# Kernel tuning notes

Hardware: AMD Instinct MI355X
Metric: run time of the kernel (lower is better)

The kernel has to match this reference:

```python
import jax, jax.numpy as jnp
import numpy as np

B, S, D, DFF = 4, 2048, 1024, 4096


def setup_inputs() -> dict:
    key = jax.random.key(0)
    ks = jax.random.split(key, 7)
    scale = 1.0 / np.sqrt(D)
    return {
        "x": jax.random.normal(ks[0], (B, S, D), dtype=jnp.float32),
        "wq": jax.random.normal(ks[1], (D, D), dtype=jnp.float32) * scale,
        "wk": jax.random.normal(ks[2], (D, D), dtype=jnp.float32) * scale,
        "wv": jax.random.normal(ks[3], (D, D), dtype=jnp.float32) * scale,
        "wo": jax.random.normal(ks[4], (D, D), dtype=jnp.float32) * scale,
        "w1": jax.random.normal(ks[5], (D, DFF), dtype=jnp.float32) * scale,
        "w2": jax.random.normal(ks[6], (DFF, D), dtype=jnp.float32) * (1.0 / np.sqrt(DFF)),
    }


def reference(x, wq, wk, wv, wo, w1, w2):
    # Single-head attention, NO 1/sqrt(d) scaling (faithful to source).
    q = x @ wq  # [B,S,D]
    k = x @ wk
    v = x @ wv
    scores = jnp.einsum("bsd,btd->bst", q, k)  # [B,S,S]
    weights = jax.nn.softmax(scores, axis=-1)
    attn = jnp.einsum("bst,btd->bsd", weights, v)
    proj = attn @ wo
    hidden = jax.nn.relu(proj @ w1)  # [B,S,DFF]
    out = hidden @ w2
    return out + x
```

## Files before the change

### kernel.cpp

```cpp
#include <hip/hip_runtime.h>
#include <hip/hip_bf16.h>
#include <hip/hip_fp16.h>


typedef _Float16 f16;
typedef __attribute__((ext_vector_type(8))) _Float16 f16x8;
typedef __attribute__((ext_vector_type(4))) _Float16 f16x4;
typedef __attribute__((ext_vector_type(4))) float f32x4;

#define BM 128
#define BN 128
#define BK 64

__device__ inline void gload16(const void* g, void* l) {
    __builtin_amdgcn_global_load_lds(
        (const __attribute__((address_space(1))) void*)g,
        (__attribute__((address_space(3))) void*)l, 16, 0, 0);
}

template<int EPI>
__global__ __launch_bounds__(256, 2)
void gemm_f16(const f16* __restrict__ A, const f16* __restrict__ Bt,
              const float* __restrict__ Res, void* __restrict__ Cv,
              int K, int lda, int ldb, int ldc,
              long long sA, long long sB, long long sC)
{
    __shared__ char smem[32 * 1024];
    f16* Ash = (f16*)smem;
    f16* Bsh = (f16*)(smem + 16384);
    float* xbuf = (float*)smem;

    const int t = threadIdx.x;
    const int z = blockIdx.z;
    A  += (size_t)z * sA;
    Bt += (size_t)z * sB;

    const int bm0 = blockIdx.x * BM;
    const int bn0 = blockIdx.y * BN;

    const int lane = t & 63;
    const int wid  = t >> 6;
    const int quad = lane >> 4;
    const int m16  = lane & 15;
    const int ks   = wid & 1;
    const int wn64 = (wid >> 1) * 64;

    const int r0 = t >> 3;
    const int kc = ((t & 7) ^ (r0 & 7)) * 8;
    const char* gA[4]; const char* gB[4];
    #pragma unroll
    for (int i = 0; i < 4; ++i) {
        gA[i] = (const char*)(A  + (size_t)(bm0 + i * 32 + r0) * lda + kc);
        gB[i] = (const char*)(Bt + (size_t)(bn0 + i * 32 + r0) * ldb + kc);
    }
    char* lA = (char*)Ash + (wid << 10);
    char* lB = (char*)Bsh + (wid << 10);

    f32x4 acc[8][4] = {};

    const int nk = K / BK;
    #define ISSUE(kt) do { const int ko = (kt) * 128;   \
        gload16(gA[0] + ko, lA);                        \
        gload16(gA[1] + ko, lA + 4096);                 \
        gload16(gA[2] + ko, lA + 8192);                 \
        gload16(gA[3] + ko, lA + 12288);                \
        gload16(gB[0] + ko, lB);                        \
        gload16(gB[1] + ko, lB + 4096);                 \
        gload16(gB[2] + ko, lB + 8192);                 \
        gload16(gB[3] + ko, lB + 12288); } while (0)

    const int swz = m16 & 7;
    const int ha  = ((ks * 4 + quad) ^ swz) * 8;

    ISSUE(0);
    for (int kt = 0; kt < nk; ++kt) {
        __syncthreads();
        f16x8 af[8], bf[4];
        #pragma unroll
        for (int i = 0; i < 8; ++i)
            af[i] = *(const f16x8*)&Ash[(i * 16 + m16) * BK + ha];
        #pragma unroll
        for (int j = 0; j < 4; ++j)
            bf[j] = *(const f16x8*)&Bsh[(wn64 + j * 16 + m16) * BK + ha];
        __syncthreads();
        if (kt + 1 < nk) ISSUE(kt + 1);
        #pragma unroll
        for (int i = 0; i < 8; ++i)
            #pragma unroll
            for (int j = 0; j < 4; ++j)
                acc[i][j] = __builtin_amdgcn_mfma_f32_16x16x32_f16(
                                af[i], bf[j], acc[i][j], 0, 0, 0);
    }
    #undef ISSUE

    float* xb = xbuf + (wid >> 1) * 4096;
    #define XIDX(row, col) ((row) * 64 + ((col) ^ (((row) & 4) << 2)))
    if (ks == 1) {
        #pragma unroll
        for (int i = 0; i < 4; ++i)
            #pragma unroll
            for (int j = 0; j < 4; ++j)
                #pragma unroll
                for (int ri = 0; ri < 4; ++ri)
                    xb[XIDX(i * 16 + quad * 4 + ri, j * 16 + m16)] = acc[i][j][ri];
    }
    __syncthreads();
    if (ks == 0) {
        #pragma unroll
        for (int i = 0; i < 4; ++i)
            #pragma unroll
            for (int j = 0; j < 4; ++j)
                #pragma unroll
                for (int ri = 0; ri < 4; ++ri)
                    acc[i][j][ri] += xb[XIDX(i * 16 + quad * 4 + ri, j * 16 + m16)];
    }
    __syncthreads();
    if (ks == 0) {
        #pragma unroll
        for (int i = 0; i < 4; ++i)
            #pragma unroll
            for (int j = 0; j < 4; ++j)
                #pragma unroll
                for (int ri = 0; ri < 4; ++ri)
                    xb[XIDX(i * 16 + quad * 4 + ri, j * 16 + m16)] = acc[i + 4][j][ri];
    }
    __syncthreads();
    if (ks == 1) {
        #pragma unroll
        for (int i = 0; i < 4; ++i)
            #pragma unroll
            for (int j = 0; j < 4; ++j)
                #pragma unroll
                for (int ri = 0; ri < 4; ++ri)
                    acc[i + 4][j][ri] += xb[XIDX(i * 16 + quad * 4 + ri, j * 16 + m16)];
    }
    #undef XIDX

    #define STORE_TILE(IB, RB)                                                  \
        do {                                                                    \
            float* C = (float*)Cv + (size_t)z * sC;                             \
            _Pragma("unroll")                                                   \
            for (int i = 0; i < 4; ++i)                                         \
                _Pragma("unroll")                                               \
                for (int ri = 0; ri < 4; ++ri) {                                \
                    const size_t row = (size_t)(bm0 + (RB) + i * 16 + quad * 4 + ri); \
                    float* cp = C + row * ldc + (bn0 + wn64 + m16);             \
                    const float* rp = Res + row * ldc + (bn0 + wn64 + m16);     \
                    _Pragma("unroll")                                           \
                    for (int j = 0; j < 4; ++j) {                               \
                        float v = acc[(IB) + i][j][ri];                         \
                        if (EPI == 3) v += rp[j * 16];                          \
                        cp[j * 16] = v;                                         \
                    }                                                           \
                }                                                               \
        } while (0)

    if (ks == 0) STORE_TILE(0, 0);
    else         STORE_TILE(4, 64);
    #undef STORE_TILE
}

template<int EPI>
__global__ __launch_bounds__(256, 2)
void gemm_ns2(const f16* __restrict__ A, const f16* __restrict__ Bt,
              void* __restrict__ Cv,
              int K, int lda, int ldb, int ldc,
              long long sA, long long sB, long long sC)
{
    __shared__ f16 Ash[BM * BK];
    __shared__ f16 Bsh[BN * BK];

    const int t = threadIdx.x;
    const int z = blockIdx.z;
    A  += (size_t)z * sA;
    Bt += (size_t)z * sB;

    const int bm0 = blockIdx.x * BM;
    const int bn0 = blockIdx.y * BN;

    const int lane = t & 63;
    const int wid  = t >> 6;
    const int quad = lane >> 4;
    const int m16  = lane & 15;
    const int wm = (wid & 1) * 64;
    const int wn = (wid >> 1) * 64;

    const int r0 = t >> 3;
    const int kc = ((t & 7) ^ (r0 & 7)) * 8;
    const char* gA[4]; const char* gB[4];
    #pragma unroll
    for (int i = 0; i < 4; ++i) {
        gA[i] = (const char*)(A  + (size_t)(bm0 + i * 32 + r0) * lda + kc);
        gB[i] = (const char*)(Bt + (size_t)(bn0 + i * 32 + r0) * ldb + kc);
    }
    char* lA = (char*)Ash + (wid << 10);
    char* lB = (char*)Bsh + (wid << 10);

    f32x4 acc[4][4] = {};

    const int nk = K / BK;
    #define ISSUE(kt) do { const int ko = (kt) * 128;   \
        gload16(gA[0] + ko, lA);                        \
        gload16(gA[1] + ko, lA + 4096);                 \
        gload16(gA[2] + ko, lA + 8192);                 \
        gload16(gA[3] + ko, lA + 12288);                \
        gload16(gB[0] + ko, lB);                        \
        gload16(gB[1] + ko, lB + 4096);                 \
        gload16(gB[2] + ko, lB + 8192);                 \
        gload16(gB[3] + ko, lB + 12288); } while (0)

    const int swz = m16 & 7;

    ISSUE(0);
    for (int kt = 0; kt < nk; ++kt) {
        __syncthreads();
        f16x8 af[2][4], bf[2][4];
        #pragma unroll
        for (int s = 0; s < 2; ++s) {
            const int ha = (((s << 2) | quad) ^ swz) * 8;
            #pragma unroll
            for (int i = 0; i < 4; ++i) {
                af[s][i] = *(const f16x8*)&Ash[(wm + i * 16 + m16) * BK + ha];
                bf[s][i] = *(const f16x8*)&Bsh[(wn + i * 16 + m16) * BK + ha];
            }
        }
        __syncthreads();
        if (kt + 1 < nk) ISSUE(kt + 1);
        #pragma unroll
        for (int s = 0; s < 2; ++s)
            #pragma unroll
            for (int i = 0; i < 4; ++i)
                #pragma unroll
                for (int j = 0; j < 4; ++j)
                    acc[i][j] = __builtin_amdgcn_mfma_f32_16x16x32_f16(
                                    af[s][i], bf[s][j], acc[i][j], 0, 0, 0);
    }
    #undef ISSUE

    if (EPI <= 1) {
        f16* C = (f16*)Cv + (size_t)z * sC;
        #pragma unroll
        for (int i = 0; i < 4; ++i)
            #pragma unroll
            for (int ri = 0; ri < 4; ++ri) {
                const size_t row = (size_t)(bm0 + wm + i * 16 + quad * 4 + ri);
                f16* cp = C + row * ldc + (bn0 + wn + m16);
                #pragma unroll
                for (int j = 0; j < 4; ++j) {
                    float v = acc[i][j][ri];
                    if (EPI == 1) v = fmaxf(v, 0.0f);
                    cp[j * 16] = (f16)v;
                }
            }
    } else {
        float* C = (float*)Cv + (size_t)z * sC;
        #pragma unroll
        for (int i = 0; i < 4; ++i)
            #pragma unroll
            for (int ri = 0; ri < 4; ++ri) {
                const size_t row = (size_t)(bm0 + wm + i * 16 + quad * 4 + ri);
                float* cp = C + row * ldc + (bn0 + wn + m16);
                #pragma unroll
                for (int j = 0; j < 4; ++j)
                    cp[j * 16] = acc[i][j][ri];
            }
    }
}

__global__ __launch_bounds__(256, 2)
void gemm_dd(const f16* __restrict__ A0, const f16* __restrict__ B0, f16* __restrict__ C0,
             const f16* __restrict__ A1, const f16* __restrict__ B1, f16* __restrict__ C1)
{
    const int LD = 1024;
    __shared__ char smem[32 * 1024];
    f16* Ash = (f16*)smem;
    f16* Bsh = (f16*)(smem + 16384);
    float* xred = (float*)smem;

    const int t = threadIdx.x;
    const int z = blockIdx.z;
    const f16* A = z ? A1 : A0;
    const f16* B = z ? B1 : B0;
    f16* C = z ? C1 : C0;

    const int bm0 = blockIdx.x * 64;
    const int bn0 = blockIdx.y * 64;

    const int lane = t & 63;
    const int wid  = t >> 6;
    const int quad = lane >> 4;
    const int m16  = lane & 15;

    const int rr = t >> 4;
    const int kc = ((t & 15) ^ (rr & 15)) * 8;
    const char* gA[4]; const char* gB[4];
    #pragma unroll
    for (int i = 0; i < 4; ++i) {
        gA[i] = (const char*)(A + (size_t)(bm0 + i * 16 + rr) * LD + kc);
        gB[i] = (const char*)(B + (size_t)(bn0 + i * 16 + rr) * LD + kc);
    }
    char* lA = (char*)Ash + (wid << 10);
    char* lB = (char*)Bsh + (wid << 10);

    f32x4 acc[4][4] = {};

    #define ISSUE(kt) do { const int ko = (kt) * 256;   \
        gload16(gA[0] + ko, lA);                        \
        gload16(gA[1] + ko, lA + 4096);                 \
        gload16(gA[2] + ko, lA + 8192);                 \
        gload16(gA[3] + ko, lA + 12288);                \
        gload16(gB[0] + ko, lB);                        \
        gload16(gB[1] + ko, lB + 4096);                 \
        gload16(gB[2] + ko, lB + 8192);                 \
        gload16(gB[3] + ko, lB + 12288); } while (0)

    const int sl = ((wid * 4 + quad) ^ m16) * 8;

    ISSUE(0);
    for (int kt = 0; kt < 8; ++kt) {
        __syncthreads();
        f16x8 af[4], bf[4];
        #pragma unroll
        for (int i = 0; i < 4; ++i) {
            af[i] = *(const f16x8*)&Ash[(i * 16 + m16) * 128 + sl];
            bf[i] = *(const f16x8*)&Bsh[(i * 16 + m16) * 128 + sl];
        }
        __syncthreads();
        if (kt + 1 < 8) ISSUE(kt + 1);
        #pragma unroll
        for (int i = 0; i < 4; ++i)
            #pragma unroll
            for (int j = 0; j < 4; ++j)
                acc[i][j] = __builtin_amdgcn_mfma_f32_16x16x32_f16(
                                af[i], bf[j], acc[i][j], 0, 0, 0);
    }
    #undef ISSUE

    #define XIDX(row, col) ((row) * 64 + ((col) ^ (((row) & 4) << 2)))
    #define WR(base) do {                                                       \
        _Pragma("unroll")                                                       \
        for (int i = 0; i < 4; ++i)                                             \
            _Pragma("unroll")                                                   \
            for (int j = 0; j < 4; ++j)                                         \
                _Pragma("unroll")                                               \
                for (int ri = 0; ri < 4; ++ri)                                  \
                    (base)[XIDX(i * 16 + quad * 4 + ri, j * 16 + m16)] = acc[i][j][ri]; \
        } while (0)
    #define RD(base) do {                                                       \
        _Pragma("unroll")                                                       \
        for (int i = 0; i < 4; ++i)                                             \
            _Pragma("unroll")                                                   \
            for (int j = 0; j < 4; ++j)                                         \
                _Pragma("unroll")                                               \
                for (int ri = 0; ri < 4; ++ri)                                  \
                    acc[i][j][ri] += (base)[XIDX(i * 16 + quad * 4 + ri, j * 16 + m16)]; \
        } while (0)

    __syncthreads();
    if (wid == 2) WR(xred);
    if (wid == 3) WR(xred + 4096);
    __syncthreads();
    if (wid == 0) RD(xred);
    if (wid == 1) RD(xred + 4096);
    __syncthreads();
    if (wid == 1) WR(xred);
    __syncthreads();
    if (wid == 0) {
        RD(xred);
        #pragma unroll
        for (int i = 0; i < 4; ++i)
            #pragma unroll
            for (int ri = 0; ri < 4; ++ri) {
                const size_t row = (size_t)(bm0 + i * 16 + quad * 4 + ri);
                f16* cp = C + row * LD + (bn0 + m16);
                #pragma unroll
                for (int j = 0; j < 4; ++j)
                    cp[j * 16] = (f16)acc[i][j][ri];
            }
    }
    #undef WR
    #undef RD
    #undef XIDX
}

__global__ __launch_bounds__(256)
void transpose_all(const float* __restrict__ wo, const float* __restrict__ w1,
                   const float* __restrict__ w2,
                   f16* __restrict__ woT, f16* __restrict__ w1T,
                   f16* __restrict__ w2T)
{
    const int z = blockIdx.z;
    const float* in; f16* out; int R, C, gx, gy;
    if (z == 0)      { in = wo; out = woT; R = 1024; C = 1024; gx = 16; gy = 16; }
    else if (z == 1) { in = w1; out = w1T; R = 1024; C = 4096; gx = 64; gy = 16; }
    else             { in = w2; out = w2T; R = 4096; C = 1024; gx = 16; gy = 64; }
    if (blockIdx.x >= (unsigned)gx || blockIdx.y >= (unsigned)gy) return;

    __shared__ float tile[64][65];
    const int c0 = blockIdx.x * 64, r0 = blockIdx.y * 64;
    const int tc = threadIdx.x & 63, tr = threadIdx.x >> 6;
    #pragma unroll
    for (int i = 0; i < 16; ++i)
        tile[tr + i * 4][tc] = in[(size_t)(r0 + tr + i * 4) * C + c0 + tc];
    __syncthreads();
    #pragma unroll
    for (int i = 0; i < 16; ++i)
        out[(size_t)(c0 + tr + i * 4) * R + r0 + tc] = (f16)tile[tc][tr + i * 4];
}

__global__ __launch_bounds__(256)
void cast_all(const float* __restrict__ x, const float* __restrict__ wq,
              const float* __restrict__ wk, const float* __restrict__ wv,
              f16* __restrict__ xh, f16* __restrict__ wqh,
              f16* __restrict__ wkh, f16* __restrict__ wvh)
{
    const int z = blockIdx.z;
    const float* in; f16* out; unsigned nblk;
    if (z == 0)      { in = x;  out = xh;  nblk = 8192; }
    else if (z == 1) { in = wq; out = wqh; nblk = 1024; }
    else if (z == 2) { in = wk; out = wkh; nblk = 1024; }
    else             { in = wv; out = wvh; nblk = 1024; }
    if (blockIdx.x >= nblk) return;
    const size_t i = ((size_t)blockIdx.x * 256 + threadIdx.x) * 4;
    float4 v = *(const float4*)(in + i);
    f16x4 o; o.x = (f16)v.x; o.y = (f16)v.y; o.z = (f16)v.z; o.w = (f16)v.w;
    *(f16x4*)(out + i) = o;
}

__global__ __launch_bounds__(256)
void softmax_f16(float* __restrict__ S)
{
    __shared__ float red[256];
    float* p = S + (size_t)blockIdx.x * 2048;
    f16* q = (f16*)p;
    const int t = threadIdx.x;

    float4 u0 = *(const float4*)(p + t * 4);
    float4 u1 = *(const float4*)(p + 1024 + t * 4);

    float m = fmaxf(fmaxf(fmaxf(u0.x, u0.y), fmaxf(u0.z, u0.w)),
                    fmaxf(fmaxf(u1.x, u1.y), fmaxf(u1.z, u1.w)));
    red[t] = m;
    __syncthreads();
    #pragma unroll
    for (int s = 128; s > 0; s >>= 1) {
        if (t < s) red[t] = fmaxf(red[t], red[t + s]);
        __syncthreads();
    }
    const float rowmax = red[0];
    __syncthreads();

    u0.x = __expf(u0.x - rowmax); u0.y = __expf(u0.y - rowmax);
    u0.z = __expf(u0.z - rowmax); u0.w = __expf(u0.w - rowmax);
    u1.x = __expf(u1.x - rowmax); u1.y = __expf(u1.y - rowmax);
    u1.z = __expf(u1.z - rowmax); u1.w = __expf(u1.w - rowmax);

    red[t] = (u0.x + u0.y + u0.z + u0.w) + (u1.x + u1.y + u1.z + u1.w);
    __syncthreads();
    #pragma unroll
    for (int s = 128; s > 0; s >>= 1) {
        if (t < s) red[t] += red[t + s];
        __syncthreads();
    }
    const float inv = 1.0f / red[0];
    __syncthreads();

    f16x4 o0, o1;
    o0.x = (f16)(u0.x * inv); o0.y = (f16)(u0.y * inv);
    o0.z = (f16)(u0.z * inv); o0.w = (f16)(u0.w * inv);
    o1.x = (f16)(u1.x * inv); o1.y = (f16)(u1.y * inv);
    o1.z = (f16)(u1.z * inv); o1.w = (f16)(u1.w * inv);
    *(f16x4*)(q + t * 4)        = o0;
    *(f16x4*)(q + 1024 + t * 4) = o1;
}

extern "C" void kernel_launch(void* const* d_in, const int* in_sizes, int n_in,
                              void* d_out, int out_size, void* d_ws, size_t ws_size,
                              hipStream_t stream)
{
    const float* x  = (const float*)d_in[0];
    const float* wq = (const float*)d_in[1];
    const float* wk = (const float*)d_in[2];
    const float* wv = (const float*)d_in[3];
    const float* wo = (const float*)d_in[4];
    const float* w1 = (const float*)d_in[5];
    const float* w2 = (const float*)d_in[6];
    float* out = (float*)d_out;

    const int S = 2048, D = 1024, DFF = 4096, Bb = 4;
    const int NTOK = Bb * S;
    const size_t M1 = 1024 * 1024;

    f16* W    = (f16*)d_ws;
    f16* xh   = W;
    f16* wqh  = W + 8 * M1;
    f16* wkh  = W + 9 * M1;
    f16* wvh  = W + 10 * M1;
    f16* woT  = W + 11 * M1;
    f16* w1T  = W + 12 * M1;
    f16* w2T  = W + 16 * M1;
    f16* wqkT = W + 20 * M1;
    f16* wvoT = W + 21 * M1;
    f16* qp   = W + 22 * M1;
    f16* vwT  = W + 30 * M1;
    float* sb = (float*)(W + 38 * M1);
    f16* ph   = (f16*)sb;
    f16* pj   = xh;
    f16* hd   = qp;

    dim3 blk(256);

    cast_all<<<dim3(NTOK * D / 1024, 1, 4), blk, 0, stream>>>(
        x, wq, wk, wv, xh, wqh, wkh, wvh);
    transpose_all<<<dim3(64, 64, 3), blk, 0, stream>>>(
        wo, w1, w2, woT, w1T, w2T);
    gemm_dd<<<dim3(16, 16, 2), blk, 0, stream>>>(
        wkh, wqh, wqkT, woT, wvh, wvoT);

    gemm_ns2<0><<<dim3(NTOK / BM, D / BN, 1), blk, 0, stream>>>(
        xh, wqkT, qp, D, D, D, D, 0, 0, 0);
    gemm_ns2<0><<<dim3(D / BM, NTOK / BN, 1), blk, 0, stream>>>(
        wvoT, xh, vwT, D, D, D, NTOK, 0, 0, 0);

    gemm_ns2<2><<<dim3(S / BM, S / BN, Bb), blk, 0, stream>>>(
        qp, xh, sb, D, D, D, S,
        (long long)S * D, (long long)S * D, (long long)S * S);

    softmax_f16<<<dim3(NTOK), blk, 0, stream>>>(sb);

    gemm_ns2<0><<<dim3(S / BM, D / BN, Bb), blk, 0, stream>>>(
        ph, vwT, pj, S, 4096, NTOK, D,
        (long long)S * 4096, (long long)S, (long long)S * D);

    gemm_ns2<1><<<dim3(NTOK / BM, DFF / BN, 1), blk, 0, stream>>>(
        pj, w1T, hd, D, D, D, DFF, 0, 0, 0);

    gemm_f16<3><<<dim3(NTOK / BM, D / BN, 1), blk, 0, stream>>>(
        hd, w2T, x, out, DFF, DFF, DFF, D, 0, 0, 0);
}
```

Before: 421.2 us.

## Merge Q/V projection GEMMs, shuffle-reduce softmax, read f16 residual

Result: faster. 409.9 us, median of 2 (-2.7%).

```diff
diff --git a/kernel.cpp b/kernel.cpp
--- a/kernel.cpp
+++ b/kernel.cpp
@@ -21,9 +21,8 @@
 template<int EPI>
 __global__ __launch_bounds__(256, 2)
 void gemm_f16(const f16* __restrict__ A, const f16* __restrict__ Bt,
-              const float* __restrict__ Res, void* __restrict__ Cv,
-              int K, int lda, int ldb, int ldc,
-              long long sA, long long sB, long long sC)
+              const f16* __restrict__ Res, float* __restrict__ C,
+              int K, int lda, int ldb, int ldc)
 {
     __shared__ char smem[32 * 1024];
     f16* Ash = (f16*)smem;
@@ -31,10 +30,6 @@
     float* xbuf = (float*)smem;
 
     const int t = threadIdx.x;
-    const int z = blockIdx.z;
-    A  += (size_t)z * sA;
-    Bt += (size_t)z * sB;
-
     const int bm0 = blockIdx.x * BM;
     const int bn0 = blockIdx.y * BN;
 
@@ -138,18 +133,17 @@
 
     #define STORE_TILE(IB, RB)                                                  \
         do {                                                                    \
-            float* C = (float*)Cv + (size_t)z * sC;                             \
             _Pragma("unroll")                                                   \
             for (int i = 0; i < 4; ++i)                                         \
                 _Pragma("unroll")                                               \
                 for (int ri = 0; ri < 4; ++ri) {                                \
                     const size_t row = (size_t)(bm0 + (RB) + i * 16 + quad * 4 + ri); \
                     float* cp = C + row * ldc + (bn0 + wn64 + m16);             \
-                    const float* rp = Res + row * ldc + (bn0 + wn64 + m16);     \
+                    const f16* rp = Res + row * ldc + (bn0 + wn64 + m16);       \
                     _Pragma("unroll")                                           \
                     for (int j = 0; j < 4; ++j) {                               \
                         float v = acc[(IB) + i][j][ri];                         \
-                        if (EPI == 3) v += rp[j * 16];                          \
+                        if (EPI == 3) v += (float)rp[j * 16];                   \
                         cp[j * 16] = v;                                         \
                     }                                                           \
                 }                                                               \
@@ -265,6 +259,94 @@
                     cp[j * 16] = acc[i][j][ri];
             }
     }
+}
+
+__global__ __launch_bounds__(256, 2)
+void gemm_qv(const f16* __restrict__ xh, const f16* __restrict__ wqkT,
+             const f16* __restrict__ wvoT,
+             f16* __restrict__ qp, f16* __restrict__ vwT)
+{
+    __shared__ f16 Ash[BM * BK];
+    __shared__ f16 Bsh[BN * BK];
+
+    const int t = threadIdx.x;
+    const int z = blockIdx.z;
+    const f16* A  = z ? wvoT : xh;
+    const f16* Bt = z ? xh   : wqkT;
+    f16* C        = z ? vwT  : qp;
+    const int lda = 1024, ldb = 1024;
+    const int ldc = z ? 8192 : 1024;
+    const int bm0 = (z ? blockIdx.y : blockIdx.x) * BM;
+    const int bn0 = (z ? blockIdx.x : blockIdx.y) * BN;
+
+    const int lane = t & 63;
+    const int wid  = t >> 6;
+    const int quad = lane >> 4;
+    const int m16  = lane & 15;
+    const int wm = (wid & 1) * 64;
+    const int wn = (wid >> 1) * 64;
+
+    const int r0 = t >> 3;
+    const int kc = ((t & 7) ^ (r0 & 7)) * 8;
+    const char* gA[4]; const char* gB[4];
+    #pragma unroll
+    for (int i = 0; i < 4; ++i) {
+        gA[i] = (const char*)(A  + (size_t)(bm0 + i * 32 + r0) * lda + kc);
+        gB[i] = (const char*)(Bt + (size_t)(bn0 + i * 32 + r0) * ldb + kc);
+    }
+    char* lA = (char*)Ash + (wid << 10);
+    char* lB = (char*)Bsh + (wid << 10);
+
+    f32x4 acc[4][4] = {};
+
+    #define ISSUE(kt) do { const int ko = (kt) * 128;   \
+        gload16(gA[0] + ko, lA);                        \
+        gload16(gA[1] + ko, lA + 4096);                 \
+        gload16(gA[2] + ko, lA + 8192);                 \
+        gload16(gA[3] + ko, lA + 12288);                \
+        gload16(gB[0] + ko, lB);                        \
+        gload16(gB[1] + ko, lB + 4096);                 \
+        gload16(gB[2] + ko, lB + 8192);                 \
+        gload16(gB[3] + ko, lB + 12288); } while (0)
+
+    const int swz = m16 & 7;
+
+    ISSUE(0);
+    for (int kt = 0; kt < 16; ++kt) {
+        __syncthreads();
+        f16x8 af[2][4], bf[2][4];
+        #pragma unroll
+        for (int s = 0; s < 2; ++s) {
+            const int ha = (((s << 2) | quad) ^ swz) * 8;
+            #pragma unroll
+            for (int i = 0; i < 4; ++i) {
+                af[s][i] = *(const f16x8*)&Ash[(wm + i * 16 + m16) * BK + ha];
+                bf[s][i] = *(const f16x8*)&Bsh[(wn + i * 16 + m16) * BK + ha];
+            }
+        }
+        __syncthreads();
+        if (kt + 1 < 16) ISSUE(kt + 1);
+        #pragma unroll
+        for (int s = 0; s < 2; ++s)
+            #pragma unroll
+            for (int i = 0; i < 4; ++i)
+                #pragma unroll
+                for (int j = 0; j < 4; ++j)
+                    acc[i][j] = __builtin_amdgcn_mfma_f32_16x16x32_f16(
+                                    af[s][i], bf[s][j], acc[i][j], 0, 0, 0);
+    }
+    #undef ISSUE
+
+    #pragma unroll
+    for (int i = 0; i < 4; ++i)
+        #pragma unroll
+        for (int ri = 0; ri < 4; ++ri) {
+            const size_t row = (size_t)(bm0 + wm + i * 16 + quad * 4 + ri);
+            f16* cp = C + row * ldc + (bn0 + wn + m16);
+            #pragma unroll
+            for (int j = 0; j < 4; ++j)
+                cp[j * 16] = (f16)acc[i][j][ri];
+        }
 }
 
 __global__ __launch_bounds__(256, 2)
@@ -430,40 +512,37 @@
 __global__ __launch_bounds__(256)
 void softmax_f16(float* __restrict__ S)
 {
-    __shared__ float red[256];
+    __shared__ float redm[4], reds[4];
     float* p = S + (size_t)blockIdx.x * 2048;
     f16* q = (f16*)p;
     const int t = threadIdx.x;
+    const int lane = t & 63, wid = t >> 6;
 
     float4 u0 = *(const float4*)(p + t * 4);
     float4 u1 = *(const float4*)(p + 1024 + t * 4);
 
     float m = fmaxf(fmaxf(fmaxf(u0.x, u0.y), fmaxf(u0.z, u0.w)),
                     fmaxf(fmaxf(u1.x, u1.y), fmaxf(u1.z, u1.w)));
-    red[t] = m;
-    __syncthreads();
-    #pragma unroll
-    for (int s = 128; s > 0; s >>= 1) {
-        if (t < s) red[t] = fmaxf(red[t], red[t + s]);
-        __syncthreads();
-    }
-    const float rowmax = red[0];
-    __syncthreads();
+    #pragma unroll
+    for (int off = 32; off > 0; off >>= 1)
+        m = fmaxf(m, __shfl_xor(m, off));
+    if (lane == 0) redm[wid] = m;
+    __syncthreads();
+    const float rowmax = fmaxf(fmaxf(redm[0], redm[1]),
+                               fmaxf(redm[2], redm[3]));
 
     u0.x = __expf(u0.x - rowmax); u0.y = __expf(u0.y - rowmax);
     u0.z = __expf(u0.z - rowmax); u0.w = __expf(u0.w - rowmax);
     u1.x = __expf(u1.x - rowmax); u1.y = __expf(u1.y - rowmax);
     u1.z = __expf(u1.z - rowmax); u1.w = __expf(u1.w - rowmax);
 
-    red[t] = (u0.x + u0.y + u0.z + u0.w) + (u1.x + u1.y + u1.z + u1.w);
-    __syncthreads();
-    #pragma unroll
-    for (int s = 128; s > 0; s >>= 1) {
-        if (t < s) red[t] += red[t + s];
-        __syncthreads();
-    }
-    const float inv = 1.0f / red[0];
-    __syncthreads();
+    float s = (u0.x + u0.y + u0.z + u0.w) + (u1.x + u1.y + u1.z + u1.w);
+    #pragma unroll
+    for (int off = 32; off > 0; off >>= 1)
+        s += __shfl_xor(s, off);
+    if (lane == 0) reds[wid] = s;
+    __syncthreads();
+    const float inv = 1.0f / (reds[0] + reds[1] + reds[2] + reds[3]);
 
     f16x4 o0, o1;
     o0.x = (f16)(u0.x * inv); o0.y = (f16)(u0.y * inv);
@@ -505,8 +584,8 @@
     f16* vwT  = W + 30 * M1;
     float* sb = (float*)(W + 38 * M1);
     f16* ph   = (f16*)sb;
-    f16* pj   = xh;
-    f16* hd   = qp;
+    f16* pj   = qp;
+    f16* hd   = W + 38 * M1;
 
     dim3 blk(256);
 
@@ -517,10 +596,8 @@
     gemm_dd<<<dim3(16, 16, 2), blk, 0, stream>>>(
         wkh, wqh, wqkT, woT, wvh, wvoT);
 
-    gemm_ns2<0><<<dim3(NTOK / BM, D / BN, 1), blk, 0, stream>>>(
-        xh, wqkT, qp, D, D, D, D, 0, 0, 0);
-    gemm_ns2<0><<<dim3(D / BM, NTOK / BN, 1), blk, 0, stream>>>(
-        wvoT, xh, vwT, D, D, D, NTOK, 0, 0, 0);
+    gemm_qv<<<dim3(NTOK / BM, D / BN, 2), blk, 0, stream>>>(
+        xh, wqkT, wvoT, qp, vwT);
 
     gemm_ns2<2><<<dim3(S / BM, S / BN, Bb), blk, 0, stream>>>(
         qp, xh, sb, D, D, D, S,
@@ -536,5 +613,5 @@
         pj, w1T, hd, D, D, D, DFF, 0, 0, 0);
 
     gemm_f16<3><<<dim3(NTOK / BM, D / BN, 1), blk, 0, stream>>>(
-        hd, w2T, x, out, DFF, DFF, DFF, D, 0, 0, 0);
-}
+        hd, w2T, xh, out, DFF, DFF, DFF, D);
+}
```
